# Kernel optimization log

Measured on AMD Instinct MI355X. Metric: run time of the kernel, lower is better.

## Reference

```python
import jax, jax.numpy as jnp
import numpy as np

# dims (match init_kwargs)
S = 2048      # sequence_length
H = 2048      # hidden_size
NH = 32       # num_attention_heads
KVH = 8       # num_key_value_heads
HD = 64       # head_dim
WIN = 128     # sliding_window
QM = NH // KVH
SM_SCALE = 1.0 / float(np.sqrt(HD))


def _rope_rotate(x, cos, sin):
    # x: [S, n, HD]; cos/sin: [S, HD//2]
    x1, x2 = jnp.split(x, 2, axis=-1)
    c = cos[:, None, :].astype(x.dtype)
    s = sin[:, None, :].astype(x.dtype)
    return jnp.concatenate([x1 * c - x2 * s, x2 * c + x1 * s], axis=-1)


def setup_inputs() -> dict:
    key = jax.random.key(0)
    ks = jax.random.split(key, 6)
    x = jax.random.normal(ks[0], (S, H), jnp.float32)
    qkv_dim = HD * (NH + 2 * KVH)
    qkv_kernel = jax.random.normal(ks[1], (H, qkv_dim), jnp.float32) * 0.02
    qkv_bias = jnp.zeros((qkv_dim,), jnp.float32)
    out_kernel = jax.random.normal(ks[2], (NH * HD, H), jnp.float32) * 0.02
    out_bias = jnp.zeros((H,), jnp.float32)
    sinks = jax.random.normal(ks[3], (NH,), jnp.float32) * 0.02
    # RoPE tables: [S, HD//2]
    pos = np.arange(S, dtype=np.float32)
    inv_freq = 1.0 / (10000.0 ** (np.arange(HD // 2, dtype=np.float32) / (HD // 2)))
    ang = pos[:, None] * inv_freq[None, :]
    cos_table = jnp.asarray(np.cos(ang), jnp.float32)
    sin_table = jnp.asarray(np.sin(ang), jnp.float32)
    # causal + sliding-window additive mask [S, S]
    qi = np.arange(S, dtype=np.int32)[:, None]
    ki = np.arange(S, dtype=np.int32)[None, :]
    m = np.where(ki > qi, -np.inf, 0.0).astype(np.float32)
    m = np.where(ki < qi - WIN, -np.inf, m).astype(np.float32)
    mask = jnp.asarray(m)
    return {"x": x, "qkv_kernel": qkv_kernel, "qkv_bias": qkv_bias,
            "out_kernel": out_kernel, "out_bias": out_bias, "sinks": sinks,
            "cos_table": cos_table, "sin_table": sin_table, "mask": mask}


def reference(x, qkv_kernel, qkv_bias, out_kernel, out_bias, sinks, cos_table, sin_table, mask):
    xf = x.astype(jnp.float32)
    qkv = jnp.dot(xf, qkv_kernel, precision=jax.lax.Precision.HIGHEST) + qkv_bias  # [S, qkv_dim]
    q_end = NH * HD
    k_end = q_end + KVH * HD
    q = qkv[:, :q_end].reshape(S, NH, HD)          # NH = KVH*QM
    k = qkv[:, q_end:k_end].reshape(S, KVH, HD)
    v = qkv[:, k_end:].reshape(S, KVH, HD)
    q = _rope_rotate(q, cos_table, sin_table).reshape(S, KVH, QM, HD)
    k = _rope_rotate(k, cos_table, sin_table)
    # logits: [KVH, QM, S_q, S_k]; K broadcast across q_mult (GQA)
    logits = jnp.einsum('qhmd,khd->hmqk', q, k) * jnp.float32(SM_SCALE)
    logits = logits + mask[None, None, :, :]
    sink = jnp.broadcast_to(sinks.reshape(KVH, QM, 1, 1).astype(jnp.float32), (KVH, QM, S, 1))
    extended = jnp.concatenate([logits, sink], axis=-1)
    weights = jax.nn.softmax(extended, axis=-1)[..., :-1]
    attn = jnp.einsum('hmqk,khd->qhmd', weights, v).reshape(S, NH * HD)
    out = jnp.dot(attn, out_kernel, precision=jax.lax.Precision.HIGHEST) + out_bias
    return out.astype(x.dtype)
```

## Files before the change

### kernel.cpp

```cpp
#include <hip/hip_runtime.h>
#include <hip/hip_bf16.h>
#include <cstdint>

typedef __hip_bfloat16 bf16;
typedef __attribute__((ext_vector_type(8))) __bf16 bf16x8;
typedef __attribute__((ext_vector_type(4))) float f32x4;

static __device__ __forceinline__ void gload_lds16(const void* g, void* l) {
  __builtin_amdgcn_global_load_lds(
      (const __attribute__((address_space(1))) uint32_t*)g,
      (__attribute__((address_space(3))) uint32_t*)l, 16, 0, 0);
}

__global__ __launch_bounds__(256)
void prep_kernel(const float* __restrict__ x, const float* __restrict__ w1,
                 const float* __restrict__ w2, bf16* __restrict__ xb,
                 bf16* __restrict__ w1t, bf16* __restrict__ w2t) {
  __shared__ float tile[32][33];
  const int lin = blockIdx.x;
  const int t = threadIdx.x;
  if (lin < 4096) {
    const int i = lin * 256 + t;
    const float4 v = reinterpret_cast<const float4*>(x)[i];
    ushort4 o;
    o.x = __builtin_bit_cast(unsigned short, __float2bfloat16(v.x));
    o.y = __builtin_bit_cast(unsigned short, __float2bfloat16(v.y));
    o.z = __builtin_bit_cast(unsigned short, __float2bfloat16(v.z));
    o.w = __builtin_bit_cast(unsigned short, __float2bfloat16(v.w));
    reinterpret_cast<ushort4*>(xb)[i] = o;
    return;
  }
  const float* in;
  bf16* out;
  int R, C, bx, by;
  if (lin < 10240) {
    const int tl = lin - 4096;
    in = w1; out = w1t; R = 2048; C = 3072; bx = tl % 96; by = tl / 96;
  } else {
    const int tl = lin - 10240;
    in = w2; out = w2t; R = 2048; C = 2048; bx = tl & 63; by = tl >> 6;
  }
  const int c0 = bx * 32, r0 = by * 32;
  const int tx = t & 31, ty = t >> 5;
#pragma unroll
  for (int i = 0; i < 4; ++i)
    tile[ty + i * 8][tx] = in[(size_t)(r0 + ty + i * 8) * C + c0 + tx];
  __syncthreads();
#pragma unroll
  for (int i = 0; i < 4; ++i)
    out[(size_t)(c0 + ty + i * 8) * R + r0 + tx] = __float2bfloat16(tile[tx][ty + i * 8]);
}

__global__ __launch_bounds__(512, 1)
void gemm1_kernel(const bf16* __restrict__ A, const bf16* __restrict__ Bt,
                  const float* __restrict__ bias,
                  bf16* __restrict__ qb, bf16* __restrict__ kb, bf16* __restrict__ vt) {
  extern __shared__ __align__(16) char smem[];
  constexpr int K = 2048, NK = 32;
  const int lin = blockIdx.x;
  const int wgid = (lin & 7) * 32 + (lin >> 3);
  const int bx = wgid >> 4, by = wgid & 15;
  const int brow = by * 128, bcol = bx * 192;
  const int t = threadIdx.x, lane = t & 63, w = t >> 6;
  const int wr = w >> 2, wc = w & 3;
  const int rr = lane & 15, rg = lane >> 4;

  char* Ab = smem;
  char* Bb = smem + 49152;

  auto stageA = [&](int kt) {
#pragma unroll
    for (int p = 0; p < 2; ++p) {
      const int idx = p * 512 + t;
      const int row = idx >> 3;
      const int cg = (idx & 7) ^ (row & 7);
      gload_lds16(A + (size_t)(brow + row) * K + kt * 64 + cg * 8,
                  Ab + (size_t)(kt % 3) * 16384 + (p * 512 + (t & ~63)) * 16);
    }
  };
  auto stageB = [&](int kt) {
#pragma unroll
    for (int p = 0; p < 3; ++p) {
      const int idx = p * 512 + t;
      const int row = idx >> 3;
      const int cg = (idx & 7) ^ (row & 7);
      gload_lds16(Bt + (size_t)(bcol + row) * K + kt * 64 + cg * 8,
                  Bb + (size_t)(kt % 3) * 24576 + (p * 512 + (t & ~63)) * 16);
    }
  };

  f32x4 acc[4][3];
#pragma unroll
  for (int i = 0; i < 4; ++i)
#pragma unroll
    for (int j = 0; j < 3; ++j) acc[i][j] = f32x4{0.f, 0.f, 0.f, 0.f};

  stageA(0); stageB(0); stageA(1); stageB(1);
  asm volatile("s_waitcnt vmcnt(5)" ::: "memory");
  __builtin_amdgcn_s_barrier();

  for (int kt = 0; kt < NK; ++kt) {
    const char* Ar = Ab + (size_t)(kt % 3) * 16384;
    const char* Br = Bb + (size_t)(kt % 3) * 24576;
#pragma unroll
    for (int ks = 0; ks < 2; ++ks) {
      bf16x8 af[4], bfr[3];
      const int c = ks * 4 + rg;
#pragma unroll
      for (int i = 0; i < 4; ++i) {
        const int row = wr * 64 + i * 16 + rr;
        af[i] = *reinterpret_cast<const bf16x8*>(Ar + row * 128 + ((c ^ (row & 7)) * 16));
      }
#pragma unroll
      for (int j = 0; j < 3; ++j) {
        const int row = wc * 48 + j * 16 + rr;
        bfr[j] = *reinterpret_cast<const bf16x8*>(Br + row * 128 + ((c ^ (row & 7)) * 16));
      }
      if (kt + 2 < NK) {
        if (ks == 0) stageA(kt + 2);
        else         stageB(kt + 2);
      }
      asm volatile("s_waitcnt lgkmcnt(0)" ::: "memory");
      __builtin_amdgcn_sched_barrier(0);
      __builtin_amdgcn_s_setprio(1);
#pragma unroll
      for (int i = 0; i < 4; ++i)
#pragma unroll
        for (int j = 0; j < 3; ++j)
          acc[i][j] = __builtin_amdgcn_mfma_f32_16x16x32_bf16(af[i], bfr[j], acc[i][j], 0, 0, 0);
      __builtin_amdgcn_s_setprio(0);
    }
    if (kt + 2 < NK)      asm volatile("s_waitcnt vmcnt(5)" ::: "memory");
    else if (kt + 1 < NK) asm volatile("s_waitcnt vmcnt(0)" ::: "memory");
    if (kt + 1 < NK) __builtin_amdgcn_s_barrier();
  }

#pragma unroll
  for (int j = 0; j < 3; ++j) {
    const int gcf = bcol + wc * 48 + j * 16;
    const int gc = gcf + rr;
    const float bv = bias[gc];
    if (gcf < 2048) {
#pragma unroll
      for (int i = 0; i < 4; ++i) {
        const int s0 = brow + wr * 64 + i * 16 + rg * 4;
#pragma unroll
        for (int r = 0; r < 4; ++r)
          qb[(size_t)(s0 + r) * 2048 + gc] = __float2bfloat16(acc[i][j][r] + bv);
      }
    } else if (gcf < 2560) {
      const int kc = gc - 2048;
#pragma unroll
      for (int i = 0; i < 4; ++i) {
        const int s0 = brow + wr * 64 + i * 16 + rg * 4;
#pragma unroll
        for (int r = 0; r < 4; ++r)
          kb[(size_t)(s0 + r) * 512 + kc] = __float2bfloat16(acc[i][j][r] + bv);
      }
    } else {
      const int vcol = gc - 2560;
#pragma unroll
      for (int i = 0; i < 4; ++i) {
        ushort4 o;
        o.x = __builtin_bit_cast(unsigned short, __float2bfloat16(acc[i][j][0] + bv));
        o.y = __builtin_bit_cast(unsigned short, __float2bfloat16(acc[i][j][1] + bv));
        o.z = __builtin_bit_cast(unsigned short, __float2bfloat16(acc[i][j][2] + bv));
        o.w = __builtin_bit_cast(unsigned short, __float2bfloat16(acc[i][j][3] + bv));
        *reinterpret_cast<ushort4*>(
            &vt[(size_t)vcol * 2048 + brow + wr * 64 + i * 16 + rg * 4]) = o;
      }
    }
  }
}

__global__ __launch_bounds__(512, 1)
void gemm2_kernel(const bf16* __restrict__ A, const bf16* __restrict__ Bt,
                  const float* __restrict__ bias, float* __restrict__ C) {
  extern __shared__ __align__(16) char smem[];
  constexpr int K = 2048, NK = 32;
  const int lin = blockIdx.x;
  const int wgid = (lin & 7) * 32 + (lin >> 3);
  const int bx = wgid >> 4, by = wgid & 15;
  const int brow = by * 128, bcol = bx * 128;
  const int t = threadIdx.x, lane = t & 63, w = t >> 6;
  const int wr = w & 3, wc = w >> 2;
  const int rr = lane & 15, rg = lane >> 4;

  char* Ab = smem;
  char* Bb = smem + 49152;

  auto stage = [&](int kt) {
#pragma unroll
    for (int p = 0; p < 2; ++p) {
      const int idx = p * 512 + t;
      const int row = idx >> 3;
      const int cg = (idx & 7) ^ (row & 7);
      gload_lds16(A + (size_t)(brow + row) * K + kt * 64 + cg * 8,
                  Ab + (size_t)(kt % 3) * 16384 + (p * 512 + (t & ~63)) * 16);
      gload_lds16(Bt + (size_t)(bcol + row) * K + kt * 64 + cg * 8,
                  Bb + (size_t)(kt % 3) * 16384 + (p * 512 + (t & ~63)) * 16);
    }
  };

  f32x4 acc[2][4];
#pragma unroll
  for (int i = 0; i < 2; ++i)
#pragma unroll
    for (int j = 0; j < 4; ++j) acc[i][j] = f32x4{0.f, 0.f, 0.f, 0.f};

  stage(0); stage(1);
  asm volatile("s_waitcnt vmcnt(4)" ::: "memory");
  __builtin_amdgcn_s_barrier();

  for (int kt = 0; kt < NK; ++kt) {
    const char* Ar = Ab + (size_t)(kt % 3) * 16384;
    const char* Br = Bb + (size_t)(kt % 3) * 16384;
#pragma unroll
    for (int ks = 0; ks < 2; ++ks) {
      bf16x8 af[2], bfr[4];
      const int c = ks * 4 + rg;
#pragma unroll
      for (int i = 0; i < 2; ++i) {
        const int row = wr * 32 + i * 16 + rr;
        af[i] = *reinterpret_cast<const bf16x8*>(Ar + row * 128 + ((c ^ (row & 7)) * 16));
      }
#pragma unroll
      for (int j = 0; j < 4; ++j) {
        const int row = wc * 64 + j * 16 + rr;
        bfr[j] = *reinterpret_cast<const bf16x8*>(Br + row * 128 + ((c ^ (row & 7)) * 16));
      }
      if (kt + 2 < NK && ks == 0) stage(kt + 2);
      asm volatile("s_waitcnt lgkmcnt(0)" ::: "memory");
      __builtin_amdgcn_sched_barrier(0);
      __builtin_amdgcn_s_setprio(1);
#pragma unroll
      for (int i = 0; i < 2; ++i)
#pragma unroll
        for (int j = 0; j < 4; ++j)
          acc[i][j] = __builtin_amdgcn_mfma_f32_16x16x32_bf16(af[i], bfr[j], acc[i][j], 0, 0, 0);
      __builtin_amdgcn_s_setprio(0);
    }
    if (kt + 2 < NK)      asm volatile("s_waitcnt vmcnt(4)" ::: "memory");
    else if (kt + 1 < NK) asm volatile("s_waitcnt vmcnt(0)" ::: "memory");
    if (kt + 1 < NK) __builtin_amdgcn_s_barrier();
  }

#pragma unroll
  for (int i = 0; i < 2; ++i)
#pragma unroll
    for (int j = 0; j < 4; ++j) {
      const int gc = bcol + wc * 64 + j * 16 + rr;
      const float bv = bias[gc];
      const int r0 = brow + wr * 32 + i * 16 + rg * 4;
#pragma unroll
      for (int r = 0; r < 4; ++r)
        C[(size_t)(r0 + r) * 2048 + gc] = acc[i][j][r] + bv;
    }
}

__global__ __launch_bounds__(256, 2)
void attn_kernel(const bf16* __restrict__ Q, const bf16* __restrict__ Kb,
                 const bf16* __restrict__ Vt, const float* __restrict__ sinks,
                 const float* __restrict__ cosT, const float* __restrict__ sinT,
                 bf16* __restrict__ aout) {
  extern __shared__ __align__(16) char smem[];
  const int hk = blockIdx.x;
  const int q0 = blockIdx.y * 32;
  const int k0 = q0 - 128;
  const int t = threadIdx.x, w = t >> 6, lane = t & 63;
  const int cl = lane & 15, rg = lane >> 4;
  const int head = hk * 4 + w;

  char* Ks = smem;
  char* Vs = smem;
  char* Ps = smem + 20480 + w * 12288;

#pragma unroll
  for (int p = 0; p < 5; ++p) {
    const int idx = p * 256 + t;
    const int row = idx >> 3, c = idx & 7;
    int key = k0 + row;
    if (key < 0) key = 0;
    gload_lds16(Kb + (size_t)key * 512 + hk * 64 + ((c ^ (row & 7)) << 3),
                Ks + (size_t)(p * 256 + (t & ~63)) * 16);
  }

  bf16x8 aq[2][2];
#pragma unroll
  for (int qf = 0; qf < 2; ++qf) {
    const int qrow = q0 + qf * 16 + cl;
    const bf16* qp = Q + (size_t)qrow * 2048 + head * 64 + rg * 8;
    const bf16x8 q1 = *reinterpret_cast<const bf16x8*>(qp);
    const bf16x8 q2 = *reinterpret_cast<const bf16x8*>(qp + 32);
    const float4 c0 = *reinterpret_cast<const float4*>(&cosT[qrow * 32 + rg * 8]);
    const float4 c1 = *reinterpret_cast<const float4*>(&cosT[qrow * 32 + rg * 8 + 4]);
    const float4 s0 = *reinterpret_cast<const float4*>(&sinT[qrow * 32 + rg * 8]);
    const float4 s1 = *reinterpret_cast<const float4*>(&sinT[qrow * 32 + rg * 8 + 4]);
    const float cs[8] = {c0.x, c0.y, c0.z, c0.w, c1.x, c1.y, c1.z, c1.w};
    const float sn[8] = {s0.x, s0.y, s0.z, s0.w, s1.x, s1.y, s1.z, s1.w};
#pragma unroll
    for (int e = 0; e < 8; ++e) {
      const float x1 = (float)q1[e], x2 = (float)q2[e];
      aq[qf][0][e] = (__bf16)(x1 * cs[e] - x2 * sn[e]);
      aq[qf][1][e] = (__bf16)(x2 * cs[e] + x1 * sn[e]);
    }
  }
  __syncthreads();

#pragma unroll
  for (int p = 0; p < 3; ++p) {
    const int task = p * 256 + t;
    if (task < 640) {
      const int row = task >> 2, c = task & 3;
      int key = k0 + row;
      if (key < 0) key = 0;
      char* base = Ks + row * 128;
      const int slotA = (c ^ (row & 7)) << 4;
      const int slotB = ((c + 4) ^ (row & 7)) << 4;
      bf16x8 v1 = *reinterpret_cast<bf16x8*>(base + slotA);
      bf16x8 v2 = *reinterpret_cast<bf16x8*>(base + slotB);
      const float4 ca0 = *reinterpret_cast<const float4*>(&cosT[key * 32 + c * 8]);
      const float4 ca1 = *reinterpret_cast<const float4*>(&cosT[key * 32 + c * 8 + 4]);
      const float4 sa0 = *reinterpret_cast<const float4*>(&sinT[key * 32 + c * 8]);
      const float4 sa1 = *reinterpret_cast<const float4*>(&sinT[key * 32 + c * 8 + 4]);
      const float cs[8] = {ca0.x, ca0.y, ca0.z, ca0.w, ca1.x, ca1.y, ca1.z, ca1.w};
      const float sn[8] = {sa0.x, sa0.y, sa0.z, sa0.w, sa1.x, sa1.y, sa1.z, sa1.w};
      bf16x8 o1, o2;
#pragma unroll
      for (int e = 0; e < 8; ++e) {
        const float x1 = (float)v1[e], x2 = (float)v2[e];
        o1[e] = (__bf16)(x1 * cs[e] - x2 * sn[e]);
        o2[e] = (__bf16)(x2 * cs[e] + x1 * sn[e]);
      }
      *reinterpret_cast<bf16x8*>(base + slotA) = o1;
      *reinterpret_cast<bf16x8*>(base + slotB) = o2;
    }
  }
  __syncthreads();

  f32x4 acc[2][10];
#pragma unroll
  for (int qf = 0; qf < 2; ++qf)
#pragma unroll
    for (int nf = 0; nf < 10; ++nf) acc[qf][nf] = f32x4{0.f, 0.f, 0.f, 0.f};

#pragma unroll
  for (int nf = 0; nf < 10; ++nf) {
    const int row = nf * 16 + cl;
    bf16x8 bk[2];
#pragma unroll
    for (int ks = 0; ks < 2; ++ks) {
      const int chunk = ks * 4 + rg;
      bk[ks] = *reinterpret_cast<const bf16x8*>(
          Ks + row * 128 + ((chunk ^ (row & 7)) << 4));
    }
#pragma unroll
    for (int qf = 0; qf < 2; ++qf)
#pragma unroll
      for (int ks = 0; ks < 2; ++ks)
        acc[qf][nf] = __builtin_amdgcn_mfma_f32_16x16x32_bf16(aq[qf][ks], bk[ks], acc[qf][nf], 0, 0, 0);
  }

  __syncthreads();

  {
    const bf16* vbase = Vt + (size_t)hk * 64 * 2048;
#pragma unroll
    for (int p = 0; p < 5; ++p) {
      const int idx = p * 256 + t;
      const int row = idx / 20;
      const int slot = idx - row * 20;
      int src = slot - (row & 7);
      if (src < 0) src += 20;
      int key = k0 + src * 8;
      if (key < 0) key = 0;
      gload_lds16(vbase + (size_t)row * 2048 + key,
                  Vs + (size_t)(p * 256 + (t & ~63)) * 16);
    }
  }

  const float sinkv = sinks[head];
  const float scale = 0.125f;
  const int cfloor = 128 - q0;
#pragma unroll
  for (int qf = 0; qf < 2; ++qf)
#pragma unroll
    for (int r = 0; r < 4; ++r) {
      const int rowb = qf * 16 + rg * 4 + r;
      int cmin = rowb;
      if (cfloor > cmin) cmin = cfloor;
      const int cmax = rowb + 128;
      float m = sinkv;
      float pv[10];
#pragma unroll
      for (int nf = 0; nf < 10; ++nf) {
        const int cc = nf * 16 + cl;
        float lv = (cc >= cmin && cc <= cmax) ? acc[qf][nf][r] * scale : -INFINITY;
        pv[nf] = lv;
        m = fmaxf(m, lv);
      }
#pragma unroll
      for (int off = 1; off < 16; off <<= 1)
        m = fmaxf(m, __shfl_xor(m, off, 64));
      float sum = 0.f;
#pragma unroll
      for (int nf = 0; nf < 10; ++nf) {
        const float p = __expf(pv[nf] - m);
        pv[nf] = p;
        sum += p;
      }
#pragma unroll
      for (int off = 1; off < 16; off <<= 1)
        sum += __shfl_xor(sum, off, 64);
      sum += __expf(sinkv - m);
      const float inv = 1.f / sum;
#pragma unroll
      for (int nf = 0; nf < 10; ++nf) {
        const int col = nf * 16 + cl;
        const int chunk = col >> 3;
        *reinterpret_cast<bf16*>(Ps + rowb * 384 + ((chunk ^ (rowb & 7)) << 4) + (cl & 7) * 2) =
            __float2bfloat16(pv[nf] * inv);
      }
    }

  asm volatile("s_waitcnt vmcnt(0) lgkmcnt(0)" ::: "memory");
  __builtin_amdgcn_sched_barrier(0);
  __syncthreads();

  f32x4 oacc[2][4];
#pragma unroll
  for (int qf = 0; qf < 2; ++qf)
#pragma unroll
    for (int j = 0; j < 4; ++j) oacc[qf][j] = f32x4{0.f, 0.f, 0.f, 0.f};

#pragma unroll
  for (int ks = 0; ks < 5; ++ks) {
    bf16x8 pa[2];
#pragma unroll
    for (int qf = 0; qf < 2; ++qf) {
      const int row = qf * 16 + cl;
      const int chunk = ks * 4 + rg;
      pa[qf] = *reinterpret_cast<const bf16x8*>(
          Ps + row * 384 + ((chunk ^ (row & 7)) << 4));
    }
#pragma unroll
    for (int j = 0; j < 4; ++j) {
      const int d = j * 16 + cl;
      int slot = ks * 4 + rg + (d & 7);
      if (slot >= 20) slot -= 20;
      const bf16x8 bv = *reinterpret_cast<const bf16x8*>(Vs + d * 320 + slot * 16);
#pragma unroll
      for (int qf = 0; qf < 2; ++qf)
        oacc[qf][j] = __builtin_amdgcn_mfma_f32_16x16x32_bf16(pa[qf], bv, oacc[qf][j], 0, 0, 0);
    }
  }

#pragma unroll
  for (int qf = 0; qf < 2; ++qf)
#pragma unroll
    for (int j = 0; j < 4; ++j)
#pragma unroll
      for (int r = 0; r < 4; ++r) {
        const int row = qf * 16 + rg * 4 + r;
        const int colb = (j * 16 + cl) * 2;
        *reinterpret_cast<bf16*>(Ps + row * 384 + (colb ^ ((row & 7) << 4))) =
            __float2bfloat16(oacc[qf][j][r]);
      }
  __syncthreads();

#pragma unroll
  for (int p = 0; p < 4; ++p) {
    const int idx = p * 256 + t;
    const int row = idx >> 5;
    const int j16 = idx & 31;
    const int w2 = j16 >> 3, c8 = j16 & 7;
    const uint4 v = *reinterpret_cast<const uint4*>(
        smem + 20480 + w2 * 12288 + row * 384 + ((c8 * 16) ^ ((row & 7) << 4)));
    *reinterpret_cast<uint4*>(aout + (size_t)(q0 + row) * 2048 + hk * 256 + j16 * 8) = v;
  }
}

extern "C" void kernel_launch(void* const* d_in, const int* in_sizes, int n_in,
                              void* d_out, int out_size, void* d_ws, size_t ws_size,
                              hipStream_t stream) {
  const float* x     = (const float*)d_in[0];
  const float* w1    = (const float*)d_in[1];
  const float* b1    = (const float*)d_in[2];
  const float* w2    = (const float*)d_in[3];
  const float* b2    = (const float*)d_in[4];
  const float* sinks = (const float*)d_in[5];
  const float* cosT  = (const float*)d_in[6];
  const float* sinT  = (const float*)d_in[7];
  float* out = (float*)d_out;

  char* ws = (char*)d_ws;
  bf16* xb   = (bf16*)(ws);
  bf16* w1t  = (bf16*)(ws + 8388608);
  bf16* w2t  = (bf16*)(ws + 20971520);
  bf16* qbuf = (bf16*)(ws + 29360128);
  bf16* kbuf = (bf16*)(ws + 37748736);
  bf16* vt   = (bf16*)(ws + 39845888);
  bf16* attn = (bf16*)(ws + 41943040);
  (void)in_sizes; (void)n_in; (void)out_size; (void)ws_size;

  prep_kernel<<<14336, 256, 0, stream>>>(x, w1, w2, xb, w1t, w2t);
  gemm1_kernel<<<256, 512, 122880, stream>>>(xb, w1t, b1, qbuf, kbuf, vt);
  attn_kernel<<<dim3(8, 64), 256, 69632, stream>>>(qbuf, kbuf, vt, sinks, cosT, sinT, attn);
  gemm2_kernel<<<256, 512, 98304, stream>>>(attn, w2t, b2, out);
}
```

Baseline: 84.77 us.

## Double attention query tile to 64 rows per block with 512 threads

```diff
diff --git a/kernel.cpp b/kernel.cpp
--- a/kernel.cpp
+++ b/kernel.cpp
@@ -258,37 +258,39 @@
     }
 }
 
-__global__ __launch_bounds__(256, 2)
+__global__ __launch_bounds__(512, 2)
 void attn_kernel(const bf16* __restrict__ Q, const bf16* __restrict__ Kb,
                  const bf16* __restrict__ Vt, const float* __restrict__ sinks,
                  const float* __restrict__ cosT, const float* __restrict__ sinT,
                  bf16* __restrict__ aout) {
   extern __shared__ __align__(16) char smem[];
   const int hk = blockIdx.x;
-  const int q0 = blockIdx.y * 32;
+  const int q0 = blockIdx.y * 64;
   const int k0 = q0 - 128;
   const int t = threadIdx.x, w = t >> 6, lane = t & 63;
   const int cl = lane & 15, rg = lane >> 4;
-  const int head = hk * 4 + w;
+  const int hl = w & 3, qsub = w >> 2;
+  const int head = hk * 4 + hl;
+  const int qbase = q0 + qsub * 32;
 
   char* Ks = smem;
   char* Vs = smem;
-  char* Ps = smem + 20480 + w * 12288;
-
-#pragma unroll
-  for (int p = 0; p < 5; ++p) {
-    const int idx = p * 256 + t;
+  char* Ps = smem + 24576 + w * 12288;
+
+#pragma unroll
+  for (int p = 0; p < 3; ++p) {
+    const int idx = p * 512 + t;
     const int row = idx >> 3, c = idx & 7;
     int key = k0 + row;
     if (key < 0) key = 0;
     gload_lds16(Kb + (size_t)key * 512 + hk * 64 + ((c ^ (row & 7)) << 3),
-                Ks + (size_t)(p * 256 + (t & ~63)) * 16);
+                Ks + (size_t)(p * 512 + (t & ~63)) * 16);
   }
 
   bf16x8 aq[2][2];
 #pragma unroll
   for (int qf = 0; qf < 2; ++qf) {
-    const int qrow = q0 + qf * 16 + cl;
+    const int qrow = qbase + qf * 16 + cl;
     const bf16* qp = Q + (size_t)qrow * 2048 + head * 64 + rg * 8;
     const bf16x8 q1 = *reinterpret_cast<const bf16x8*>(qp);
     const bf16x8 q2 = *reinterpret_cast<const bf16x8*>(qp + 32);
@@ -308,9 +310,9 @@
   __syncthreads();
 
 #pragma unroll
-  for (int p = 0; p < 3; ++p) {
-    const int task = p * 256 + t;
-    if (task < 640) {
+  for (int p = 0; p < 2; ++p) {
+    const int task = p * 512 + t;
+    if (task < 768) {
       const int row = task >> 2, c = task & 3;
       int key = k0 + row;
       if (key < 0) key = 0;
@@ -338,14 +340,14 @@
   }
   __syncthreads();
 
-  f32x4 acc[2][10];
+  f32x4 acc[2][12];
 #pragma unroll
   for (int qf = 0; qf < 2; ++qf)
 #pragma unroll
-    for (int nf = 0; nf < 10; ++nf) acc[qf][nf] = f32x4{0.f, 0.f, 0.f, 0.f};
-
-#pragma unroll
-  for (int nf = 0; nf < 10; ++nf) {
+    for (int nf = 0; nf < 12; ++nf) acc[qf][nf] = f32x4{0.f, 0.f, 0.f, 0.f};
+
+#pragma unroll
+  for (int nf = 0; nf < 12; ++nf) {
     const int row = nf * 16 + cl;
     bf16x8 bk[2];
 #pragma unroll
@@ -366,16 +368,16 @@
   {
     const bf16* vbase = Vt + (size_t)hk * 64 * 2048;
 #pragma unroll
-    for (int p = 0; p < 5; ++p) {
-      const int idx = p * 256 + t;
-      const int row = idx / 20;
-      const int slot = idx - row * 20;
-      int src = slot - (row & 7);
-      if (src < 0) src += 20;
+    for (int p = 0; p < 3; ++p) {
+      const int idx = p * 512 + t;
+      const int d = idx / 24;
+      const int slot = idx - d * 24;
+      int src = slot - (d & 7) * 3;
+      if (src < 0) src += 24;
       int key = k0 + src * 8;
       if (key < 0) key = 0;
-      gload_lds16(vbase + (size_t)row * 2048 + key,
-                  Vs + (size_t)(p * 256 + (t & ~63)) * 16);
+      gload_lds16(vbase + (size_t)d * 2048 + key,
+                  Vs + (size_t)(p * 512 + (t & ~63)) * 16);
     }
   }
 
@@ -386,14 +388,15 @@
   for (int qf = 0; qf < 2; ++qf)
 #pragma unroll
     for (int r = 0; r < 4; ++r) {
-      const int rowb = qf * 16 + rg * 4 + r;
+      const int roww = qf * 16 + rg * 4 + r;
+      const int rowb = qsub * 32 + roww;
       int cmin = rowb;
       if (cfloor > cmin) cmin = cfloor;
       const int cmax = rowb + 128;
       float m = sinkv;
-      float pv[10];
-#pragma unroll
-      for (int nf = 0; nf < 10; ++nf) {
+      float pv[12];
+#pragma unroll
+      for (int nf = 0; nf < 12; ++nf) {
         const int cc = nf * 16 + cl;
         float lv = (cc >= cmin && cc <= cmax) ? acc[qf][nf][r] * scale : -INFINITY;
         pv[nf] = lv;
@@ -404,7 +407,7 @@
         m = fmaxf(m, __shfl_xor(m, off, 64));
       float sum = 0.f;
 #pragma unroll
-      for (int nf = 0; nf < 10; ++nf) {
+      for (int nf = 0; nf < 12; ++nf) {
         const float p = __expf(pv[nf] - m);
         pv[nf] = p;
         sum += p;
@@ -415,10 +418,12 @@
       sum += __expf(sinkv - m);
       const float inv = 1.f / sum;
 #pragma unroll
-      for (int nf = 0; nf < 10; ++nf) {
+      for (int nf = 0; nf < 12; ++nf) {
         const int col = nf * 16 + cl;
         const int chunk = col >> 3;
-        *reinterpret_cast<bf16*>(Ps + rowb * 384 + ((chunk ^ (rowb & 7)) << 4) + (cl & 7) * 2) =
+        int slot = chunk + (roww & 7) * 3;
+        if (slot >= 24) slot -= 24;
+        *reinterpret_cast<bf16*>(Ps + roww * 384 + slot * 16 + (cl & 7) * 2) =
             __float2bfloat16(pv[nf] * inv);
       }
     }
@@ -434,21 +439,21 @@
     for (int j = 0; j < 4; ++j) oacc[qf][j] = f32x4{0.f, 0.f, 0.f, 0.f};
 
 #pragma unroll
-  for (int ks = 0; ks < 5; ++ks) {
+  for (int ks = 0; ks < 6; ++ks) {
     bf16x8 pa[2];
 #pragma unroll
     for (int qf = 0; qf < 2; ++qf) {
       const int row = qf * 16 + cl;
-      const int chunk = ks * 4 + rg;
-      pa[qf] = *reinterpret_cast<const bf16x8*>(
-          Ps + row * 384 + ((chunk ^ (row & 7)) << 4));
+      int slot = ks * 4 + rg + (row & 7) * 3;
+      if (slot >= 24) slot -= 24;
+      pa[qf] = *reinterpret_cast<const bf16x8*>(Ps + row * 384 + slot * 16);
     }
 #pragma unroll
     for (int j = 0; j < 4; ++j) {
       const int d = j * 16 + cl;
-      int slot = ks * 4 + rg + (d & 7);
-      if (slot >= 20) slot -= 20;
-      const bf16x8 bv = *reinterpret_cast<const bf16x8*>(Vs + d * 320 + slot * 16);
+      int slot = ks * 4 + rg + (d & 7) * 3;
+      if (slot >= 24) slot -= 24;
+      const bf16x8 bv = *reinterpret_cast<const bf16x8*>(Vs + d * 384 + slot * 16);
 #pragma unroll
       for (int qf = 0; qf < 2; ++qf)
         oacc[qf][j] = __builtin_amdgcn_mfma_f32_16x16x32_bf16(pa[qf], bv, oacc[qf][j], 0, 0, 0);
@@ -470,13 +475,15 @@
 
 #pragma unroll
   for (int p = 0; p < 4; ++p) {
-    const int idx = p * 256 + t;
-    const int row = idx >> 5;
+    const int idx = p * 512 + t;
+    const int rowg = idx >> 5;
     const int j16 = idx & 31;
-    const int w2 = j16 >> 3, c8 = j16 & 7;
+    const int hsrc = j16 >> 3, c8 = j16 & 7;
+    const int wsrc = (rowg >> 5) * 4 + hsrc;
+    const int row = rowg & 31;
     const uint4 v = *reinterpret_cast<const uint4*>(
-        smem + 20480 + w2 * 12288 + row * 384 + ((c8 * 16) ^ ((row & 7) << 4)));
-    *reinterpret_cast<uint4*>(aout + (size_t)(q0 + row) * 2048 + hk * 256 + j16 * 8) = v;
+        smem + 24576 + wsrc * 12288 + row * 384 + ((c8 * 16) ^ ((row & 7) << 4)));
+    *reinterpret_cast<uint4*>(aout + (size_t)(q0 + rowg) * 2048 + hk * 256 + j16 * 8) = v;
   }
 }
 
@@ -505,6 +512,6 @@
 
   prep_kernel<<<14336, 256, 0, stream>>>(x, w1, w2, xb, w1t, w2t);
   gemm1_kernel<<<256, 512, 122880, stream>>>(xb, w1t, b1, qbuf, kbuf, vt);
-  attn_kernel<<<dim3(8, 64), 256, 69632, stream>>>(qbuf, kbuf, vt, sinks, cosT, sinT, attn);
+  attn_kernel<<<dim3(8, 32), 512, 122880, stream>>>(qbuf, kbuf, vt, sinks, cosT, sinT, attn);
   gemm2_kernel<<<256, 512, 98304, stream>>>(attn, w2t, b2, out);
 }
```

New measurement: 85.97 us. About the same (+1.4%).
